# Optimization experiments

Hardware: AMD Instinct MI355X
Metric: run time of the kernel (lower is better)

Reference implementation:

```python
import jax, jax.numpy as jnp
import numpy as np

B, NQ, NK, D = 8, 2048, 2048, 256


def setup_inputs() -> dict:
    key = jax.random.key(0)
    ks = jax.random.split(key, 4)
    scale = 1.0 / np.sqrt(D)
    return {
        "query": jax.random.normal(ks[0], (B, NQ, D), dtype=jnp.float32),
        "key": jax.random.normal(ks[1], (B, NK, D), dtype=jnp.float32),
        "Wq": jax.random.normal(ks[2], (D, D), dtype=jnp.float32) * scale,
        "bq": jnp.zeros((D,), dtype=jnp.float32),
        "Wk": jax.random.normal(ks[3], (D, D), dtype=jnp.float32) * scale,
        "bk": jnp.zeros((D,), dtype=jnp.float32),
    }


def reference(query, key, Wq, bq, Wk, bk):
    # value = key (pre-projection), as in the torch module
    value = key
    # FFT over the sequence axis (dim=1), keep real part
    q = jnp.real(jnp.fft.fft(query, axis=1)).astype(query.dtype)
    # torch nn.Linear: y = x @ W.T + b
    q = q @ Wq.T + bq                      # [B, NQ, D]
    k = key @ Wk.T + bk                    # [B, NK, D]
    scale = 1.0 / jnp.sqrt(jnp.asarray(q.shape[-1], q.dtype))
    scores = jnp.einsum('bqd,bkd->bqk', q, k) * scale   # [B, NQ, NK]
    probs = jax.nn.softmax(scores, axis=-1)
    out = jnp.einsum('bqk,bkd->bqd', probs, value)       # [B, NQ, D]
    return out
```

## Files before the change

### kernel.cpp

```cpp
#include <hip/hip_runtime.h>

#define B_ 8
#define NQ_ 2048
#define NK_ 2048
#define D_ 256
#define KF_ 1056

typedef __attribute__((ext_vector_type(8))) short bf16x8_t;
typedef __attribute__((ext_vector_type(4))) float f32x4_t;

static __device__ __forceinline__ unsigned short f2bf(float x) {
  unsigned int u = __float_as_uint(x);
  unsigned int r = (u + 0x7FFFu + ((u >> 16) & 1u)) >> 16;
  return (unsigned short)r;
}
static __device__ __forceinline__ float bf2f(unsigned short b) {
  return __uint_as_float(((unsigned int)b) << 16);
}

typedef __attribute__((address_space(1))) unsigned int gas_u32;
typedef __attribute__((address_space(3))) unsigned int las_u32;
static __device__ __forceinline__ void gl16(const void* g, void* l) {
  __builtin_amdgcn_global_load_lds((const gas_u32*)g, (las_u32*)l, 16, 0, 0);
}

__global__ __launch_bounds__(256) void split_kernel(const float* __restrict__ x,
                                                    unsigned short* __restrict__ xh,
                                                    unsigned short* __restrict__ xl,
                                                    int n) {
  const int i = blockIdx.x * 256 + threadIdx.x;
  if (i < n) {
    const float v = x[i];
    const unsigned short hb = f2bf(v);
    xh[i] = hb;
    xl[i] = f2bf(v - bf2f(hb));
  }
}

__global__ __launch_bounds__(256) void cos_split_kernel(unsigned short* __restrict__ Ch,
                                                        unsigned short* __restrict__ Cl) {
  const int idx = blockIdx.x * 256 + threadIdx.x;
  const int i = idx / KF_, n = idx % KF_;
  float c = 0.f;
  if (n <= 1024) {
    const int m = (i * n) & 2047;
    c = cosf((float)m * 0.0030679615757712823f);
  }
  const unsigned short hb = f2bf(c);
  Ch[idx] = hb;
  Cl[idx] = f2bf(c - bf2f(hb));
}

__global__ __launch_bounds__(256) void qtf_split_kernel(const float* __restrict__ q,
                                                        unsigned short* __restrict__ Qtfh,
                                                        unsigned short* __restrict__ Qtfl) {
  __shared__ float lds[32][33];
  const int t  = threadIdx.x;
  const int n0 = blockIdx.x * 32;
  const int d0 = blockIdx.y * 32;
  const int b  = blockIdx.z;
#pragma unroll
  for (int p = 0; p < 4; ++p) {
    const int idx = t + 256 * p;
    const int dd = idx & 31, nn = idx >> 5;
    const int n = n0 + nn;
    float v = 0.f;
    if (n <= 1024) v = q[((size_t)b * NQ_ + n) * D_ + d0 + dd];
    if (n >= 1 && n <= 1023) v += q[((size_t)b * NQ_ + (2048 - n)) * D_ + d0 + dd];
    lds[nn][dd] = v;
  }
  __syncthreads();
#pragma unroll
  for (int p = 0; p < 4; ++p) {
    const int idx = t + 256 * p;
    const int nn = idx & 31, dd = idx >> 5;
    const float v = lds[nn][dd];
    const unsigned short hb = f2bf(v);
    const size_t o = ((size_t)b * D_ + d0 + dd) * KF_ + n0 + nn;
    Qtfh[o] = hb;
    Qtfl[o] = f2bf(v - bf2f(hb));
  }
}

__global__ __launch_bounds__(256) void vt_bf16_kernel(const unsigned short* __restrict__ keyh,
                                                      unsigned short* __restrict__ Vt) {
  __shared__ unsigned short lds[32][40];
  const int t  = threadIdx.x;
  const int j0 = blockIdx.x * 32;
  const int d0 = blockIdx.y * 32;
  const int b  = blockIdx.z;
#pragma unroll
  for (int p = 0; p < 4; ++p) {
    const int idx = t + 256 * p;
    const int dd = idx & 31, jj = idx >> 5;
    lds[jj][dd] = keyh[((size_t)b * NK_ + j0 + jj) * D_ + d0 + dd];
  }
  __syncthreads();
#pragma unroll
  for (int p = 0; p < 4; ++p) {
    const int idx = t + 256 * p;
    const int jj = idx & 31, dd = idx >> 5;
    Vt[((size_t)b * D_ + d0 + dd) * NK_ + j0 + jj] = lds[jj][dd];
  }
}

__global__ __launch_bounds__(256, 2) void dft_mfma(const unsigned short* __restrict__ Ch,
                                                   const unsigned short* __restrict__ Cl,
                                                   const unsigned short* __restrict__ Qtfh,
                                                   const unsigned short* __restrict__ Qtfl,
                                                   float* __restrict__ qr) {
  __shared__ __align__(16) unsigned short Ah[128][40];
  __shared__ __align__(16) unsigned short Al[128][40];
  __shared__ __align__(16) unsigned short Bh[128][40];
  __shared__ __align__(16) unsigned short Bl[128][40];
  const int t = threadIdx.x;
  const int b = blockIdx.z / 3, split = blockIdx.z % 3;
  const int i0 = blockIdx.x * 128, d0 = blockIdx.y * 128;
  const int w = t >> 6, lane = t & 63, quad = lane >> 4, l16 = lane & 15;
  const int wq = w & 1, wj = w >> 1;
  float* qrs = qr + (size_t)split * ((size_t)B_ * 1152 * D_);

  f32x4_t acc[4][4];
#pragma unroll
  for (int a = 0; a < 4; ++a)
#pragma unroll
    for (int c = 0; c < 4; ++c) acc[a][c] = (f32x4_t)0.f;

  const size_t abase = (size_t)i0 * KF_;
  const size_t bbase = ((size_t)b * D_ + d0) * KF_;

  for (int c0 = split * 352; c0 < split * 352 + 352; c0 += 32) {
#pragma unroll
    for (int it = 0; it < 2; ++it) {
      const int unit = t + 256 * it;
      const int row = unit >> 2, u = (unit & 3) * 8;
      const size_t go = (size_t)row * KF_ + c0 + u;
      *(uint4*)&Ah[row][u] = *(const uint4*)&Ch[abase + go];
      *(uint4*)&Al[row][u] = *(const uint4*)&Cl[abase + go];
      *(uint4*)&Bh[row][u] = *(const uint4*)&Qtfh[bbase + go];
      *(uint4*)&Bl[row][u] = *(const uint4*)&Qtfl[bbase + go];
    }
    __syncthreads();
    {
      const int dcol = quad * 8;
      bf16x8_t ah[4], al[4], bh[4], bl[4];
#pragma unroll
      for (int x = 0; x < 4; ++x) {
        ah[x] = *(const bf16x8_t*)&Ah[wq * 64 + x * 16 + l16][dcol];
        al[x] = *(const bf16x8_t*)&Al[wq * 64 + x * 16 + l16][dcol];
        bh[x] = *(const bf16x8_t*)&Bh[wj * 64 + x * 16 + l16][dcol];
        bl[x] = *(const bf16x8_t*)&Bl[wj * 64 + x * 16 + l16][dcol];
      }
#pragma unroll
      for (int at = 0; at < 4; ++at)
#pragma unroll
        for (int jt = 0; jt < 4; ++jt) {
          acc[at][jt] = __builtin_amdgcn_mfma_f32_16x16x32_bf16(ah[at], bh[jt], acc[at][jt], 0, 0, 0);
          acc[at][jt] = __builtin_amdgcn_mfma_f32_16x16x32_bf16(ah[at], bl[jt], acc[at][jt], 0, 0, 0);
          acc[at][jt] = __builtin_amdgcn_mfma_f32_16x16x32_bf16(al[at], bh[jt], acc[at][jt], 0, 0, 0);
        }
    }
    __syncthreads();
  }
#pragma unroll
  for (int at = 0; at < 4; ++at) {
#pragma unroll
    for (int jt = 0; jt < 4; ++jt) {
      const int d = d0 + wj * 64 + jt * 16 + l16;
#pragma unroll
      for (int r = 0; r < 4; ++r) {
        const int i = i0 + wq * 64 + at * 16 + quad * 4 + r;
        qrs[((size_t)b * 1152 + i) * D_ + d] = acc[at][jt][r];
      }
    }
  }
}

__global__ __launch_bounds__(256) void qr_finalize_kernel(const float* __restrict__ qr,
                                                          unsigned short* __restrict__ qrh,
                                                          unsigned short* __restrict__ qrl) {
  const int i = blockIdx.x, b = blockIdx.y, d = threadIdx.x;
  const int src = (i <= 1087) ? i : (2048 - i);
  const size_t S = (size_t)B_ * 1152 * D_;
  const size_t idx = ((size_t)b * 1152 + src) * D_ + d;
  const float v = qr[idx] + qr[idx + S] + qr[idx + 2 * S];
  const unsigned short hb = f2bf(v);
  const size_t o = ((size_t)b * NQ_ + i) * D_ + d;
  qrh[o] = hb;
  qrl[o] = f2bf(v - bf2f(hb));
}

__global__ __launch_bounds__(256, 2) void proj_mfma(const unsigned short* __restrict__ xh,
                                                    const unsigned short* __restrict__ xl,
                                                    const unsigned short* __restrict__ Wh,
                                                    const unsigned short* __restrict__ Wl,
                                                    const float* __restrict__ bias,
                                                    unsigned short* __restrict__ yh,
                                                    unsigned short* __restrict__ yl) {
  __shared__ __align__(16) unsigned short Xh[128][72];
  __shared__ __align__(16) unsigned short Xl[128][72];
  __shared__ __align__(16) unsigned short Bh[128][72];
  __shared__ __align__(16) unsigned short Bl[128][72];
  const int t = threadIdx.x;
  const int m0 = blockIdx.x * 128, o0 = blockIdx.y * 128;
  const int w = t >> 6, lane = t & 63, quad = lane >> 4, l16 = lane & 15;
  const int wq = w & 1, wj = w >> 1;

  f32x4_t acc[4][4];
#pragma unroll
  for (int a = 0; a < 4; ++a)
#pragma unroll
    for (int c = 0; c < 4; ++c) acc[a][c] = (f32x4_t)0.f;

  const size_t xbase = (size_t)m0 * D_;
  const size_t wbase = (size_t)o0 * D_;

  for (int c0 = 0; c0 < D_; c0 += 64) {
#pragma unroll
    for (int it = 0; it < 4; ++it) {
      const int unit = t + 256 * it;
      const int row = unit >> 3, u = (unit & 7) * 8;
      const size_t go = (size_t)row * D_ + c0 + u;
      *(uint4*)&Xh[row][u] = *(const uint4*)&xh[xbase + go];
      *(uint4*)&Xl[row][u] = *(const uint4*)&xl[xbase + go];
      *(uint4*)&Bh[row][u] = *(const uint4*)&Wh[wbase + go];
      *(uint4*)&Bl[row][u] = *(const uint4*)&Wl[wbase + go];
    }
    __syncthreads();
#pragma unroll
    for (int ks = 0; ks < 2; ++ks) {
      const int dcol = ks * 32 + quad * 8;
      bf16x8_t ah[4], al[4], bh[4], bl[4];
#pragma unroll
      for (int x = 0; x < 4; ++x) {
        ah[x] = *(const bf16x8_t*)&Xh[wq * 64 + x * 16 + l16][dcol];
        al[x] = *(const bf16x8_t*)&Xl[wq * 64 + x * 16 + l16][dcol];
        bh[x] = *(const bf16x8_t*)&Bh[wj * 64 + x * 16 + l16][dcol];
        bl[x] = *(const bf16x8_t*)&Bl[wj * 64 + x * 16 + l16][dcol];
      }
#pragma unroll
      for (int at = 0; at < 4; ++at)
#pragma unroll
        for (int jt = 0; jt < 4; ++jt) {
          acc[at][jt] = __builtin_amdgcn_mfma_f32_16x16x32_bf16(ah[at], bh[jt], acc[at][jt], 0, 0, 0);
          acc[at][jt] = __builtin_amdgcn_mfma_f32_16x16x32_bf16(ah[at], bl[jt], acc[at][jt], 0, 0, 0);
          acc[at][jt] = __builtin_amdgcn_mfma_f32_16x16x32_bf16(al[at], bh[jt], acc[at][jt], 0, 0, 0);
        }
    }
    __syncthreads();
  }
#pragma unroll
  for (int at = 0; at < 4; ++at) {
#pragma unroll
    for (int jt = 0; jt < 4; ++jt) {
      const int o = o0 + wj * 64 + jt * 16 + l16;
      const float bv = bias[o];
#pragma unroll
      for (int r = 0; r < 4; ++r) {
        const int m = m0 + wq * 64 + at * 16 + quad * 4 + r;
        const float v = acc[at][jt][r] + bv;
        const unsigned short hb = f2bf(v);
        yh[(size_t)m * D_ + o] = hb;
        yl[(size_t)m * D_ + o] = f2bf(v - bf2f(hb));
      }
    }
  }
}

__global__ __launch_bounds__(512, 2) void scores_p(const unsigned short* __restrict__ qh,
                                                   const unsigned short* __restrict__ ql,
                                                   const unsigned short* __restrict__ kh,
                                                   const unsigned short* __restrict__ kl,
                                                   unsigned short* __restrict__ Pb,
                                                   float2* __restrict__ stat) {
  __shared__ __align__(16) unsigned short Qh[2][128][32];
  __shared__ __align__(16) unsigned short Ql[2][128][32];
  __shared__ __align__(16) unsigned short Kh[2][128][32];
  __shared__ __align__(16) unsigned short Kl[2][128][32];
  __shared__ float mred[2][128];
  __shared__ float lred[2][128];
  const int t = threadIdx.x;
  const int b = blockIdx.z;
  const int i0 = blockIdx.x * 128, j0 = blockIdx.y * 128;
  const int jb = blockIdx.y;
  const int w = t >> 6, lane = t & 63, quad = lane >> 4, l16 = lane & 15;
  const int wq = w & 3, wj = w >> 2;
  const int srw = t >> 2, ssl = t & 3;

  f32x4_t acc[2][4];
#pragma unroll
  for (int x = 0; x < 2; ++x)
#pragma unroll
    for (int y = 0; y < 4; ++y) acc[x][y] = (f32x4_t)0.f;

  const size_t qbase = ((size_t)b * NQ_ + i0) * D_;
  const size_t kbase = ((size_t)b * NK_ + j0) * D_;

  auto STAGE = [&](int nb, int c0) {
    const int sg = (ssl ^ ((srw >> 1) & 3)) * 8;
    const size_t ro = (size_t)srw * D_ + c0 + sg;
    gl16(qh + qbase + ro, &Qh[nb][w * 16][0]);
    gl16(ql + qbase + ro, &Ql[nb][w * 16][0]);
    gl16(kh + kbase + ro, &Kh[nb][w * 16][0]);
    gl16(kl + kbase + ro, &Kl[nb][w * 16][0]);
  };

  STAGE(0, 0);

#pragma unroll
  for (int s = 0; s < 8; ++s) {
    const int cb = s & 1;
    if (s < 7) {
      STAGE(cb ^ 1, (s + 1) * 32);
      asm volatile("s_waitcnt vmcnt(4)" ::: "memory");
    } else {
      asm volatile("s_waitcnt vmcnt(0)" ::: "memory");
    }
    __builtin_amdgcn_s_barrier();
    asm volatile("" ::: "memory");

    bf16x8_t ah[2], al[2], bh[4], bl[4];
#pragma unroll
    for (int x = 0; x < 2; ++x) {
      const int ar = wq * 32 + x * 16 + l16;
      const int asl = (quad ^ ((ar >> 1) & 3)) * 8;
      ah[x] = *(const bf16x8_t*)&Qh[cb][ar][asl];
      al[x] = *(const bf16x8_t*)&Ql[cb][ar][asl];
    }
#pragma unroll
    for (int y = 0; y < 4; ++y) {
      const int br = wj * 64 + y * 16 + l16;
      const int bsl = (quad ^ ((br >> 1) & 3)) * 8;
      bh[y] = *(const bf16x8_t*)&Kh[cb][br][bsl];
      bl[y] = *(const bf16x8_t*)&Kl[cb][br][bsl];
    }
#pragma unroll
    for (int x = 0; x < 2; ++x)
#pragma unroll
      for (int y = 0; y < 4; ++y) {
        acc[x][y] = __builtin_amdgcn_mfma_f32_16x16x32_bf16(ah[x], bh[y], acc[x][y], 0, 0, 0);
        acc[x][y] = __builtin_amdgcn_mfma_f32_16x16x32_bf16(ah[x], bl[y], acc[x][y], 0, 0, 0);
        acc[x][y] = __builtin_amdgcn_mfma_f32_16x16x32_bf16(al[x], bh[y], acc[x][y], 0, 0, 0);
      }

    asm volatile("" ::: "memory");
    __builtin_amdgcn_s_barrier();
    asm volatile("" ::: "memory");
  }

  const float scale = 0.0625f;
  float mt[2][4];
#pragma unroll
  for (int x = 0; x < 2; ++x)
#pragma unroll
    for (int r = 0; r < 4; ++r) mt[x][r] = -3e38f;
#pragma unroll
  for (int x = 0; x < 2; ++x)
#pragma unroll
    for (int y = 0; y < 4; ++y)
#pragma unroll
      for (int r = 0; r < 4; ++r) {
        acc[x][y][r] *= scale;
        mt[x][r] = fmaxf(mt[x][r], acc[x][y][r]);
      }
#pragma unroll
  for (int off = 1; off < 16; off <<= 1)
#pragma unroll
    for (int x = 0; x < 2; ++x)
#pragma unroll
      for (int r = 0; r < 4; ++r) mt[x][r] = fmaxf(mt[x][r], __shfl_xor(mt[x][r], off));
  if (l16 == 0) {
#pragma unroll
    for (int x = 0; x < 2; ++x)
#pragma unroll
      for (int r = 0; r < 4; ++r)
        mred[wj][wq * 32 + x * 16 + quad * 4 + r] = mt[x][r];
  }
  __syncthreads();
  float nrow[2][4], mu[2][4], lt[2][4];
#pragma unroll
  for (int x = 0; x < 2; ++x)
#pragma unroll
    for (int r = 0; r < 4; ++r) {
      const int rr = wq * 32 + x * 16 + quad * 4 + r;
      const float m = fmaxf(mred[0][rr], mred[1][rr]);
      const float n = ceilf(m * 1.44269504f);
      nrow[x][r] = n;
      mu[x][r] = n * 0.69314718056f;
      lt[x][r] = 0.f;
    }
  const size_t pbase = ((size_t)(b * 16 + jb)) * NQ_ * 128;
#pragma unroll
  for (int x = 0; x < 2; ++x)
#pragma unroll
    for (int y = 0; y < 4; ++y) {
      const int jloc = wj * 64 + y * 16 + l16;
#pragma unroll
      for (int r = 0; r < 4; ++r) {
        const int i = i0 + wq * 32 + x * 16 + quad * 4 + r;
        float p = __expf(acc[x][y][r] - mu[x][r]);
        p = fmaxf(p, 8.673617e-19f);
        lt[x][r] += p;
        Pb[pbase + (size_t)i * 128 + jloc] = f2bf(p);
      }
    }
#pragma unroll
  for (int off = 1; off < 16; off <<= 1)
#pragma unroll
    for (int x = 0; x < 2; ++x)
#pragma unroll
      for (int r = 0; r < 4; ++r) lt[x][r] += __shfl_xor(lt[x][r], off);
  if (l16 == 0) {
#pragma unroll
    for (int x = 0; x < 2; ++x)
#pragma unroll
      for (int r = 0; r < 4; ++r)
        lred[wj][wq * 32 + x * 16 + quad * 4 + r] = lt[x][r];
  }
  __syncthreads();
  if (wj == 0 && l16 == 0) {
#pragma unroll
    for (int x = 0; x < 2; ++x)
#pragma unroll
      for (int r = 0; r < 4; ++r) {
        const int rr = wq * 32 + x * 16 + quad * 4 + r;
        stat[(size_t)jb * (B_ * NQ_) + (size_t)b * NQ_ + i0 + rr] =
            make_float2(nrow[x][r], lred[0][rr] + lred[1][rr]);
      }
  }
}

__global__ __launch_bounds__(256) void rowfin_kernel(const float2* __restrict__ stat,
                                                     float2* __restrict__ srow) {
  const int i = blockIdx.x * 256 + threadIdx.x;
  float2 st[16];
  float m = -3e38f;
#pragma unroll
  for (int jb = 0; jb < 16; ++jb) {
    st[jb] = stat[(size_t)jb * (B_ * NQ_) + i];
    m = fmaxf(m, st[jb].x);
  }
  float l = 0.f;
#pragma unroll
  for (int jb = 0; jb < 16; ++jb) l += st[jb].y * exp2f(st[jb].x - m);
  srow[i] = make_float2(m, 1.0f / l);
}

__global__ __launch_bounds__(512, 1) void pv_p(const unsigned short* __restrict__ Pb,
                                               const float2* __restrict__ stat,
                                               const float2* __restrict__ srow,
                                               const unsigned short* __restrict__ Vt,
                                               float* __restrict__ out) {
  __shared__ __align__(16) unsigned short Ps[3][64][64];
  __shared__ __align__(16) unsigned short Vs[3][256][64];
  const int t = threadIdx.x;
  const int lb = (blockIdx.x & 7) * 32 + (blockIdx.x >> 3);
  const int mb = lb * 64;
  const int b  = lb >> 5;
  const int i0 = mb & (NQ_ - 1);
  const int w = t >> 6, lane = t & 63, quad = lane >> 4, l16 = lane & 15;
  const int wm = w & 1, wd = w >> 1;
  const int prow = t >> 3, pslot = t & 7;

  unsigned int es2[16][2];
  {
    float nmax[2];
#pragma unroll
    for (int x = 0; x < 2; ++x)
      nmax[x] = srow[mb + wm * 32 + x * 16 + l16].x;
#pragma unroll
    for (int jb = 0; jb < 16; ++jb)
#pragma unroll
      for (int x = 0; x < 2; ++x) {
        const int arow = mb + wm * 32 + x * 16 + l16;
        int e = (int)(nmax[x] - stat[(size_t)jb * (B_ * NQ_) + arow].x);
        e = e < 0 ? 0 : (e > 60 ? 60 : e);
        es2[jb][x] = (unsigned int)(e << 7) * 0x00010001u;
      }
  }

  f32x4_t acc[2][4];
#pragma unroll
  for (int x = 0; x < 2; ++x)
#pragma unroll
    for (int y = 0; y < 4; ++y) acc[x][y] = (f32x4_t)0.f;

  const size_t vbase = (size_t)b * D_ * (size_t)NK_;

  auto STAGE = [&](int nb, int s) {
    const int jj = s * 64;
    const int jb = jj >> 7, off = jj & 127;
    {
      const int sg = pslot ^ (prow & 7);
      gl16(Pb + ((size_t)(b * 16 + jb)) * NQ_ * 128 +
               (size_t)(i0 + prow) * 128 + off + sg * 8,
           &Ps[nb][w * 8][0]);
    }
#pragma unroll
    for (int k = 0; k < 4; ++k) {
      const int vrow = k * 64 + prow;
      const int sg = pslot ^ (vrow & 7);
      gl16(Vt + vbase + (size_t)vrow * NK_ + jj + sg * 8,
           &Vs[nb][k * 64 + w * 8][0]);
    }
  };

  asm volatile("s_waitcnt vmcnt(0)" ::: "memory");
  STAGE(0, 0);
  STAGE(1, 1);

#pragma unroll
  for (int s = 0; s < 32; ++s) {
    const int cb = s % 3;
    if (s < 30) {
      STAGE((s + 2) % 3, s + 2);
      asm volatile("s_waitcnt vmcnt(10)" ::: "memory");
    } else if (s == 30) {
      asm volatile("s_waitcnt vmcnt(5)" ::: "memory");
    } else {
      asm volatile("s_waitcnt vmcnt(0)" ::: "memory");
    }
    __builtin_amdgcn_s_barrier();
    asm volatile("" ::: "memory");

    const unsigned int e0 = es2[s >> 1][0], e1 = es2[s >> 1][1];
#pragma unroll
    for (int ks = 0; ks < 2; ++ks) {
      bf16x8_t a[2], bv[4];
#pragma unroll
      for (int x = 0; x < 2; ++x) {
        const int row = wm * 32 + x * 16 + l16;
        const int sk = (ks * 4 + quad) ^ (row & 7);
        uint4 u = *(const uint4*)&Ps[cb][row][sk * 8];
        const unsigned int e = (x == 0) ? e0 : e1;
        u.x -= e; u.y -= e; u.z -= e; u.w -= e;
        a[x] = *(const bf16x8_t*)&u;
      }
#pragma unroll
      for (int y = 0; y < 4; ++y) {
        const int row = wd * 64 + y * 16 + l16;
        const int sk = (ks * 4 + quad) ^ (row & 7);
        bv[y] = *(const bf16x8_t*)&Vs[cb][row][sk * 8];
      }
#pragma unroll
      for (int x = 0; x < 2; ++x)
#pragma unroll
        for (int y = 0; y < 4; ++y)
          acc[x][y] = __builtin_amdgcn_mfma_f32_16x16x32_bf16(a[x], bv[y], acc[x][y], 0, 0, 0);
    }

    asm volatile("" ::: "memory");
    __builtin_amdgcn_s_barrier();
    asm volatile("" ::: "memory");
  }

#pragma unroll
  for (int x = 0; x < 2; ++x) {
    float sy[4];
#pragma unroll
    for (int r = 0; r < 4; ++r)
      sy[r] = srow[mb + wm * 32 + x * 16 + quad * 4 + r].y;
#pragma unroll
    for (int y = 0; y < 4; ++y) {
      const int d = wd * 64 + y * 16 + l16;
#pragma unroll
      for (int r = 0; r < 4; ++r) {
        const int m = mb + wm * 32 + x * 16 + quad * 4 + r;
        out[(size_t)m * D_ + d] = acc[x][y][r] * sy[r];
      }
    }
  }
}

extern "C" void kernel_launch(void* const* d_in, const int* in_sizes, int n_in,
                              void* d_out, int out_size, void* d_ws, size_t ws_size,
                              hipStream_t stream) {
  const float* query = (const float*)d_in[0];
  const float* key   = (const float*)d_in[1];
  const float* Wq    = (const float*)d_in[2];
  const float* bq    = (const float*)d_in[3];
  const float* Wk    = (const float*)d_in[4];
  const float* bk    = (const float*)d_in[5];
  float* out = (float*)d_out;

  char* ws = (char*)d_ws;
  const size_t MB = (size_t)1 << 20;
  unsigned short* qh = (unsigned short*)(ws);
  unsigned short* ql = (unsigned short*)(ws + 8 * MB);
  unsigned short* kh = (unsigned short*)(ws + 16 * MB);
  unsigned short* kl = (unsigned short*)(ws + 24 * MB);
  unsigned short* Vt = (unsigned short*)(ws + 32 * MB);
  unsigned short* Pb = (unsigned short*)(ws + 40 * MB);
  float2* stat = (float2*)(ws + 108 * MB);
  float2* srow = (float2*)(ws + 110 * MB);
  unsigned short* Ch   = (unsigned short*)(ws + 40 * MB);
  unsigned short* Cl   = (unsigned short*)(ws + 43 * MB);
  unsigned short* Qtfh = (unsigned short*)(ws + 46 * MB);
  unsigned short* Qtfl = (unsigned short*)(ws + 51 * MB);
  float*          qr   = (float*)(ws + 56 * MB);
  unsigned short* qrh  = (unsigned short*)(ws + 40 * MB);
  unsigned short* qrl  = (unsigned short*)(ws + 48 * MB);
  unsigned short* keyh = (unsigned short*)(ws + 92 * MB);
  unsigned short* keyl = (unsigned short*)(ws + 100 * MB);
  unsigned short* Wqh  = (unsigned short*)(ws + 111 * MB);
  unsigned short* Wql  = (unsigned short*)(ws + 111 * MB + 256 * 1024);
  unsigned short* Wkh  = (unsigned short*)(ws + 111 * MB + 512 * 1024);
  unsigned short* Wkl  = (unsigned short*)(ws + 111 * MB + 768 * 1024);

  dim3 blk(256);

  split_kernel<<<B_ * NK_ * D_ / 256, blk, 0, stream>>>(key, keyh, keyl, B_ * NK_ * D_);
  split_kernel<<<D_ * D_ / 256, blk, 0, stream>>>(Wq, Wqh, Wql, D_ * D_);
  split_kernel<<<D_ * D_ / 256, blk, 0, stream>>>(Wk, Wkh, Wkl, D_ * D_);
  cos_split_kernel<<<1152 * KF_ / 256, blk, 0, stream>>>(Ch, Cl);
  qtf_split_kernel<<<dim3(KF_ / 32, D_ / 32, B_), blk, 0, stream>>>(query, Qtfh, Qtfl);
  dft_mfma<<<dim3(9, 2, B_ * 3), blk, 0, stream>>>(Ch, Cl, Qtfh, Qtfl, qr);
  qr_finalize_kernel<<<dim3(2048, B_), blk, 0, stream>>>(qr, qrh, qrl);
  proj_mfma<<<dim3(B_ * NQ_ / 128, 2), blk, 0, stream>>>(qrh, qrl, Wqh, Wql, bq, qh, ql);
  proj_mfma<<<dim3(B_ * NK_ / 128, 2), blk, 0, stream>>>(keyh, keyl, Wkh, Wkl, bk, kh, kl);
  vt_bf16_kernel<<<dim3(NK_ / 32, D_ / 32, B_), blk, 0, stream>>>(keyh, Vt);
  scores_p<<<dim3(NQ_ / 128, NK_ / 128, B_), dim3(512), 0, stream>>>(qh, ql, kh, kl, Pb, stat);
  rowfin_kernel<<<B_ * NQ_ / 256, blk, 0, stream>>>(stat, srow);
  pv_p<<<dim3(256), dim3(512), 0, stream>>>(Pb, stat, srow, Vt, out);
}
```

Before: 207.4 us.

## Single-buffer scores kernel with 64-wide K chunks to raise occupancy

Changes the scores_p kernel from a double-buffered 32-column LDS pipeline to a single 64-column buffer loaded synchronously each step, with a new 8-way XOR swizzle. Launch bounds go from 2 to 4 blocks per CU. The aim is to halve the k-loop iterations and barriers and to fit more blocks per CU so the waves hide latency. In exchange, global loads no longer overlap compute inside a block and register pressure is tighter.

```diff
diff --git a/kernel.cpp b/kernel.cpp
--- a/kernel.cpp
+++ b/kernel.cpp
@@ -267,16 +267,16 @@
   }
 }
 
-__global__ __launch_bounds__(512, 2) void scores_p(const unsigned short* __restrict__ qh,
+__global__ __launch_bounds__(512, 4) void scores_p(const unsigned short* __restrict__ qh,
                                                    const unsigned short* __restrict__ ql,
                                                    const unsigned short* __restrict__ kh,
                                                    const unsigned short* __restrict__ kl,
                                                    unsigned short* __restrict__ Pb,
                                                    float2* __restrict__ stat) {
-  __shared__ __align__(16) unsigned short Qh[2][128][32];
-  __shared__ __align__(16) unsigned short Ql[2][128][32];
-  __shared__ __align__(16) unsigned short Kh[2][128][32];
-  __shared__ __align__(16) unsigned short Kl[2][128][32];
+  __shared__ __align__(16) unsigned short Qh[128][64];
+  __shared__ __align__(16) unsigned short Ql[128][64];
+  __shared__ __align__(16) unsigned short Kh[128][64];
+  __shared__ __align__(16) unsigned short Kl[128][64];
   __shared__ float mred[2][128];
   __shared__ float lred[2][128];
   const int t = threadIdx.x;
@@ -285,7 +285,7 @@
   const int jb = blockIdx.y;
   const int w = t >> 6, lane = t & 63, quad = lane >> 4, l16 = lane & 15;
   const int wq = w & 3, wj = w >> 2;
-  const int srw = t >> 2, ssl = t & 3;
+  const int sr0 = t >> 3, ssl = t & 7;
 
   f32x4_t acc[2][4];
 #pragma unroll
@@ -296,56 +296,58 @@
   const size_t qbase = ((size_t)b * NQ_ + i0) * D_;
   const size_t kbase = ((size_t)b * NK_ + j0) * D_;
 
-  auto STAGE = [&](int nb, int c0) {
-    const int sg = (ssl ^ ((srw >> 1) & 3)) * 8;
-    const size_t ro = (size_t)srw * D_ + c0 + sg;
-    gl16(qh + qbase + ro, &Qh[nb][w * 16][0]);
-    gl16(ql + qbase + ro, &Ql[nb][w * 16][0]);
-    gl16(kh + kbase + ro, &Kh[nb][w * 16][0]);
-    gl16(kl + kbase + ro, &Kl[nb][w * 16][0]);
+  auto STAGE = [&](int c0) {
+#pragma unroll
+    for (int half = 0; half < 2; ++half) {
+      const int row = half * 64 + sr0;
+      const int sg = (ssl ^ (row & 7)) * 8;
+      const size_t ro = (size_t)row * D_ + c0 + sg;
+      gl16(qh + qbase + ro, &Qh[half * 64 + w * 8][0]);
+      gl16(ql + qbase + ro, &Ql[half * 64 + w * 8][0]);
+      gl16(kh + kbase + ro, &Kh[half * 64 + w * 8][0]);
+      gl16(kl + kbase + ro, &Kl[half * 64 + w * 8][0]);
+    }
   };
 
-  STAGE(0, 0);
-
-#pragma unroll
-  for (int s = 0; s < 8; ++s) {
-    const int cb = s & 1;
-    if (s < 7) {
-      STAGE(cb ^ 1, (s + 1) * 32);
-      asm volatile("s_waitcnt vmcnt(4)" ::: "memory");
-    } else {
-      asm volatile("s_waitcnt vmcnt(0)" ::: "memory");
-    }
+  STAGE(0);
+
+#pragma unroll
+  for (int s = 0; s < 4; ++s) {
+    asm volatile("s_waitcnt vmcnt(0)" ::: "memory");
     __builtin_amdgcn_s_barrier();
     asm volatile("" ::: "memory");
 
-    bf16x8_t ah[2], al[2], bh[4], bl[4];
-#pragma unroll
-    for (int x = 0; x < 2; ++x) {
-      const int ar = wq * 32 + x * 16 + l16;
-      const int asl = (quad ^ ((ar >> 1) & 3)) * 8;
-      ah[x] = *(const bf16x8_t*)&Qh[cb][ar][asl];
-      al[x] = *(const bf16x8_t*)&Ql[cb][ar][asl];
-    }
-#pragma unroll
-    for (int y = 0; y < 4; ++y) {
-      const int br = wj * 64 + y * 16 + l16;
-      const int bsl = (quad ^ ((br >> 1) & 3)) * 8;
-      bh[y] = *(const bf16x8_t*)&Kh[cb][br][bsl];
-      bl[y] = *(const bf16x8_t*)&Kl[cb][br][bsl];
-    }
-#pragma unroll
-    for (int x = 0; x < 2; ++x)
+#pragma unroll
+    for (int ks = 0; ks < 2; ++ks) {
+      bf16x8_t ah[2], al[2], bh[4], bl[4];
+#pragma unroll
+      for (int x = 0; x < 2; ++x) {
+        const int ar = wq * 32 + x * 16 + l16;
+        const int asl = ((ks * 4 + quad) ^ (ar & 7)) * 8;
+        ah[x] = *(const bf16x8_t*)&Qh[ar][asl];
+        al[x] = *(const bf16x8_t*)&Ql[ar][asl];
+      }
 #pragma unroll
       for (int y = 0; y < 4; ++y) {
-        acc[x][y] = __builtin_amdgcn_mfma_f32_16x16x32_bf16(ah[x], bh[y], acc[x][y], 0, 0, 0);
-        acc[x][y] = __builtin_amdgcn_mfma_f32_16x16x32_bf16(ah[x], bl[y], acc[x][y], 0, 0, 0);
-        acc[x][y] = __builtin_amdgcn_mfma_f32_16x16x32_bf16(al[x], bh[y], acc[x][y], 0, 0, 0);
-      }
+        const int br = wj * 64 + y * 16 + l16;
+        const int bsl = ((ks * 4 + quad) ^ (br & 7)) * 8;
+        bh[y] = *(const bf16x8_t*)&Kh[br][bsl];
+        bl[y] = *(const bf16x8_t*)&Kl[br][bsl];
+      }
+#pragma unroll
+      for (int x = 0; x < 2; ++x)
+#pragma unroll
+        for (int y = 0; y < 4; ++y) {
+          acc[x][y] = __builtin_amdgcn_mfma_f32_16x16x32_bf16(ah[x], bh[y], acc[x][y], 0, 0, 0);
+          acc[x][y] = __builtin_amdgcn_mfma_f32_16x16x32_bf16(ah[x], bl[y], acc[x][y], 0, 0, 0);
+          acc[x][y] = __builtin_amdgcn_mfma_f32_16x16x32_bf16(al[x], bh[y], acc[x][y], 0, 0, 0);
+        }
+    }
 
     asm volatile("" ::: "memory");
     __builtin_amdgcn_s_barrier();
     asm volatile("" ::: "memory");
+    if (s < 3) STAGE((s + 1) * 64);
   }
 
   const float scale = 0.0625f;
```

After: 206.7 us. Within noise of the previous version (-0.3%).

## Triple-buffer scores staging with interleaved hi/lo bf16 tiles in LDS

Applied to the files above, without the earlier changes.

The scores kernel now stages Q and K tiles into a three-deep LDS ring instead of a double buffer, prefetching two k-steps ahead with matching vmcnt waits. The hi and lo bf16 halves are packed into a single 64-wide row per buffer with an XOR swizzle over 8 slots, in place of four separate arrays. The aim is to hide more global-load latency and keep LDS reads conflict-free. The cost is more LDS per block (about 96KB versus 64KB), which may not fit two 512-thread blocks per CU as the launch bounds request.

```diff
diff --git a/kernel.cpp b/kernel.cpp
--- a/kernel.cpp
+++ b/kernel.cpp
@@ -273,10 +273,8 @@
                                                    const unsigned short* __restrict__ kl,
                                                    unsigned short* __restrict__ Pb,
                                                    float2* __restrict__ stat) {
-  __shared__ __align__(16) unsigned short Qh[2][128][32];
-  __shared__ __align__(16) unsigned short Ql[2][128][32];
-  __shared__ __align__(16) unsigned short Kh[2][128][32];
-  __shared__ __align__(16) unsigned short Kl[2][128][32];
+  __shared__ __align__(16) unsigned short Qhl[3][128][64];
+  __shared__ __align__(16) unsigned short Khl[3][128][64];
   __shared__ float mred[2][128];
   __shared__ float lred[2][128];
   const int t = threadIdx.x;
@@ -285,7 +283,6 @@
   const int jb = blockIdx.y;
   const int w = t >> 6, lane = t & 63, quad = lane >> 4, l16 = lane & 15;
   const int wq = w & 3, wj = w >> 2;
-  const int srw = t >> 2, ssl = t & 3;
 
   f32x4_t acc[2][4];
 #pragma unroll
@@ -296,22 +293,36 @@
   const size_t qbase = ((size_t)b * NQ_ + i0) * D_;
   const size_t kbase = ((size_t)b * NK_ + j0) * D_;
 
-  auto STAGE = [&](int nb, int c0) {
-    const int sg = (ssl ^ ((srw >> 1) & 3)) * 8;
-    const size_t ro = (size_t)srw * D_ + c0 + sg;
-    gl16(qh + qbase + ro, &Qh[nb][w * 16][0]);
-    gl16(ql + qbase + ro, &Ql[nb][w * 16][0]);
-    gl16(kh + kbase + ro, &Kh[nb][w * 16][0]);
-    gl16(kl + kbase + ro, &Kl[nb][w * 16][0]);
+  auto STAGE = [&](int nb, int s) {
+    const int c0 = s * 32;
+#pragma unroll
+    for (int cp = 0; cp < 2; ++cp) {
+      const int r = w * 16 + cp * 8 + (lane >> 3);
+      const int lg = (lane & 7) ^ (r & 7);
+      const unsigned short* src = (lg < 4) ? qh : ql;
+      gl16(src + qbase + (size_t)r * D_ + c0 + (lg & 3) * 8,
+           &Qhl[nb][w * 16 + cp * 8][0]);
+    }
+#pragma unroll
+    for (int cp = 0; cp < 2; ++cp) {
+      const int r = w * 16 + cp * 8 + (lane >> 3);
+      const int lg = (lane & 7) ^ (r & 7);
+      const unsigned short* src = (lg < 4) ? kh : kl;
+      gl16(src + kbase + (size_t)r * D_ + c0 + (lg & 3) * 8,
+           &Khl[nb][w * 16 + cp * 8][0]);
+    }
   };
 
   STAGE(0, 0);
+  STAGE(1, 1);
 
 #pragma unroll
   for (int s = 0; s < 8; ++s) {
-    const int cb = s & 1;
-    if (s < 7) {
-      STAGE(cb ^ 1, (s + 1) * 32);
+    const int cb = s % 3;
+    if (s < 6) {
+      STAGE((s + 2) % 3, s + 2);
+      asm volatile("s_waitcnt vmcnt(8)" ::: "memory");
+    } else if (s == 6) {
       asm volatile("s_waitcnt vmcnt(4)" ::: "memory");
     } else {
       asm volatile("s_waitcnt vmcnt(0)" ::: "memory");
@@ -323,16 +334,14 @@
 #pragma unroll
     for (int x = 0; x < 2; ++x) {
       const int ar = wq * 32 + x * 16 + l16;
-      const int asl = (quad ^ ((ar >> 1) & 3)) * 8;
-      ah[x] = *(const bf16x8_t*)&Qh[cb][ar][asl];
-      al[x] = *(const bf16x8_t*)&Ql[cb][ar][asl];
+      ah[x] = *(const bf16x8_t*)&Qhl[cb][ar][(quad ^ (ar & 7)) * 8];
+      al[x] = *(const bf16x8_t*)&Qhl[cb][ar][((4 + quad) ^ (ar & 7)) * 8];
     }
 #pragma unroll
     for (int y = 0; y < 4; ++y) {
       const int br = wj * 64 + y * 16 + l16;
-      const int bsl = (quad ^ ((br >> 1) & 3)) * 8;
-      bh[y] = *(const bf16x8_t*)&Kh[cb][br][bsl];
-      bl[y] = *(const bf16x8_t*)&Kl[cb][br][bsl];
+      bh[y] = *(const bf16x8_t*)&Khl[cb][br][(quad ^ (br & 7)) * 8];
+      bl[y] = *(const bf16x8_t*)&Khl[cb][br][((4 + quad) ^ (br & 7)) * 8];
     }
 #pragma unroll
     for (int x = 0; x < 2; ++x)
```

Result: slower. 216.7 us (+4.5%).
